# Optimization experiments

Hardware: AMD Instinct MI355X
Metric: run time of the kernel (lower is better)

The kernel has to match this reference:

```python
import jax, jax.numpy as jnp
import numpy as np

B, D, G, K, NP = 8, 1024, 32, 64, 1024


def setup_inputs() -> dict:
    key = jax.random.key(0)
    ks = jax.random.split(key, 7)
    x = jax.random.normal(ks[0], (B, NP, D), jnp.float32)
    weights = jax.random.uniform(ks[1], (B, G), jnp.float32)
    xopt = jax.random.normal(ks[2], (B, D), jnp.float32)
    R = jax.random.normal(ks[3], (K, K), jnp.float32) / np.sqrt(K).astype(np.float32)
    group_indices = jax.random.randint(ks[4], (B, G, K), 0, D)
    valid_mask = jax.random.randint(ks[5], (B, G, K), 0, 2).astype(bool)
    group_counts = jax.random.randint(ks[6], (B,), 1, G + 1)
    return dict(x=x, weights=weights, xopt=xopt, R=R,
                group_indices=group_indices, valid_mask=valid_mask,
                group_counts=group_counts)


def reference(x, weights, xopt, R, group_indices, valid_mask, group_counts):
    Bb, NPp, Dd = x.shape
    Gg, Kk = group_indices.shape[1], group_indices.shape[2]
    # elliptic coefficients 1e6**linspace(0,1,K), a deterministic buffer
    coeffs = jnp.asarray(1.0e6, x.dtype) ** jnp.linspace(0.0, 1.0, Kk).astype(x.dtype)
    z = x - xopt[:, None, :]                                   # (B,NP,D)
    # gather per-group sub-vectors without materializing (B,G,NP,D):
    # zb: (NP,D), ib: (G,K) -> zb[:, ib]: (NP,G,K)
    z_sub = jax.vmap(lambda zb, ib: zb[:, ib])(z, group_indices)  # (B,NP,G,K)
    z_sub = jnp.transpose(z_sub, (0, 2, 1, 3))                 # (B,G,NP,K)
    # per-group small rotation
    z_rot = jnp.einsum('bgnk,kl->bgnl', z_sub, R)              # (B,G,NP,K)
    # mask invalid dims of each group, elliptic weighted sum over K
    masked_coeffs = jnp.where(valid_mask[:, :, None, :], coeffs[None, None, None, :],
                              jnp.zeros((), x.dtype))          # (B,G,NP->bcast,K)
    elliptic_vals = jnp.sum(masked_coeffs * z_rot * z_rot, axis=-1)  # (B,G,NP)
    # mask invalid groups, weighted reduce over groups
    group_valid = (jnp.arange(Gg)[None, :] < group_counts[:, None]).astype(x.dtype)  # (B,G)
    fitness = jnp.einsum('bgn,bg->bn', elliptic_vals, weights * group_valid)  # (B,NP)
    return fitness
```

## Files before the change

### kernel.cpp

```cpp
#include <hip/hip_runtime.h>

typedef _Float16 half8  __attribute__((ext_vector_type(8)));
typedef _Float16 half4h __attribute__((ext_vector_type(4)));
typedef float    f32x4  __attribute__((ext_vector_type(4)));

#define B_     8
#define D_     1024
#define G_     32
#define K_     64
#define NP_    1024
#define ROWS   32
#define TPB    1024
#define STRIDE 1028

__global__ __launch_bounds__(TPB) void fitness(
    const float* __restrict__ x,
    const float* __restrict__ weights,
    const float* __restrict__ xopt,
    const float* __restrict__ R,
    const int* __restrict__ gidx,
    const int* __restrict__ mask,
    const int* __restrict__ counts,
    float* __restrict__ out) {
  __shared__ _Float16 zh[ROWS * STRIDE];
  __shared__ int      gli[G_ * K_];
  __shared__ _Float16 Rb[8 * 512];
  __shared__ float    wcs[G_ * K_];
  __shared__ float    redrow[ROWS];

  const int tile = blockIdx.x;
  const int b    = blockIdx.y;
  const int t    = threadIdx.x;
  const int cnt  = counts[b];

  gli[t]        = gidx[b * (G_ * K_) + t];
  gli[t + 1024] = gidx[b * (G_ * K_) + 1024 + t];

  {
    const float C = 19.931568569324174f / 63.0f;
#pragma unroll
    for (int r = 0; r < 2; ++r) {
      int idx = t + r * 1024;
      int g = idx >> 6, l = idx & 63;
      bool v = (g < cnt) && (mask[b * (G_ * K_) + idx] != 0);
      wcs[idx] = v ? weights[b * G_ + g] * exp2f((float)l * C) : 0.0f;
    }
  }

  {
    int pos  = t * 4;
    int frag = pos >> 9, rem = pos & 511;
    int lane = rem >> 3, j0 = rem & 7;
    int kt = frag >> 2, nt = frag & 3;
    int quad = lane >> 4, ln = lane & 15;
    half4h rv;
#pragma unroll
    for (int e = 0; e < 4; ++e) {
      int k = kt * 32 + quad * 8 + j0 + e;
      rv[e] = (_Float16)R[k * K_ + nt * 16 + ln];
    }
    *(half4h*)(Rb + pos) = rv;
  }

  if (t < ROWS) redrow[t] = 0.0f;

  {
    const float4* x4  = (const float4*)(x + ((size_t)(b * NP_ + tile * ROWS)) * D_);
    const float4* xo4 = (const float4*)(xopt + b * D_);
    const int col4 = t & 255;
    float4 xo = xo4[col4];
#pragma unroll
    for (int j = 0; j < (ROWS * 256) / TPB; ++j) {
      int row = (t >> 8) + 4 * j;
      float4 xv = x4[row * 256 + col4];
      half4h hv;
      hv[0] = (_Float16)(xv.x - xo.x);
      hv[1] = (_Float16)(xv.y - xo.y);
      hv[2] = (_Float16)(xv.z - xo.z);
      hv[3] = (_Float16)(xv.w - xo.w);
      *(half4h*)(zh + row * STRIDE + col4 * 4) = hv;
    }
  }
  __syncthreads();

  const int wv   = t >> 6;
  const int lane = t & 63;
  const int quad = lane >> 4;
  const int ln   = lane & 15;
  const int items = 2 * cnt;

  const half8* rbf = (const half8*)Rb;

  for (int i = wv; i < items; i += 16) {
    const int g     = i >> 1;
    const int mtile = i & 1;

    const int* gp = gli + g * K_ + quad * 8;
    int4 i0 = *(const int4*)(gp);
    int4 i1 = *(const int4*)(gp + 4);
    int4 i2 = *(const int4*)(gp + 32);
    int4 i3 = *(const int4*)(gp + 36);
    const _Float16* zr = zh + (mtile * 16 + ln) * STRIDE;
    half8 a0, a1;
    a0[0] = zr[i0.x]; a0[1] = zr[i0.y]; a0[2] = zr[i0.z]; a0[3] = zr[i0.w];
    a0[4] = zr[i1.x]; a0[5] = zr[i1.y]; a0[6] = zr[i1.z]; a0[7] = zr[i1.w];
    a1[0] = zr[i2.x]; a1[1] = zr[i2.y]; a1[2] = zr[i2.z]; a1[3] = zr[i2.w];
    a1[4] = zr[i3.x]; a1[5] = zr[i3.y]; a1[6] = zr[i3.z]; a1[7] = zr[i3.w];

    f32x4 c0 = {0.f, 0.f, 0.f, 0.f}, c1 = c0, c2 = c0, c3 = c0;
    c0 = __builtin_amdgcn_mfma_f32_16x16x32_f16(a0, rbf[0 * 64 + lane], c0, 0, 0, 0);
    c1 = __builtin_amdgcn_mfma_f32_16x16x32_f16(a0, rbf[1 * 64 + lane], c1, 0, 0, 0);
    c2 = __builtin_amdgcn_mfma_f32_16x16x32_f16(a0, rbf[2 * 64 + lane], c2, 0, 0, 0);
    c3 = __builtin_amdgcn_mfma_f32_16x16x32_f16(a0, rbf[3 * 64 + lane], c3, 0, 0, 0);
    c0 = __builtin_amdgcn_mfma_f32_16x16x32_f16(a1, rbf[4 * 64 + lane], c0, 0, 0, 0);
    c1 = __builtin_amdgcn_mfma_f32_16x16x32_f16(a1, rbf[5 * 64 + lane], c1, 0, 0, 0);
    c2 = __builtin_amdgcn_mfma_f32_16x16x32_f16(a1, rbf[6 * 64 + lane], c2, 0, 0, 0);
    c3 = __builtin_amdgcn_mfma_f32_16x16x32_f16(a1, rbf[7 * 64 + lane], c3, 0, 0, 0);

    const float* wg = wcs + g * K_ + ln;
    float w0 = wg[0], w1 = wg[16], w2 = wg[32], w3 = wg[48];
    float q0, q1, q2, q3;
    q0 = w0 * c0[0] * c0[0] + w1 * c1[0] * c1[0] + w2 * c2[0] * c2[0] + w3 * c3[0] * c3[0];
    q1 = w0 * c0[1] * c0[1] + w1 * c1[1] * c1[1] + w2 * c2[1] * c2[1] + w3 * c3[1] * c3[1];
    q2 = w0 * c0[2] * c0[2] + w1 * c1[2] * c1[2] + w2 * c2[2] * c2[2] + w3 * c3[2] * c3[2];
    q3 = w0 * c0[3] * c0[3] + w1 * c1[3] * c1[3] + w2 * c2[3] * c2[3] + w3 * c3[3] * c3[3];

#pragma unroll
    for (int off = 1; off < 16; off <<= 1) {
      q0 += __shfl_xor(q0, off);
      q1 += __shfl_xor(q1, off);
      q2 += __shfl_xor(q2, off);
      q3 += __shfl_xor(q3, off);
    }
    if (ln == 0) {
      float* rr = redrow + mtile * 16 + quad * 4;
      atomicAdd(rr + 0, q0);
      atomicAdd(rr + 1, q1);
      atomicAdd(rr + 2, q2);
      atomicAdd(rr + 3, q3);
    }
  }
  __syncthreads();

  if (t < ROWS) out[b * NP_ + tile * ROWS + t] = redrow[t];
}

extern "C" void kernel_launch(void* const* d_in, const int* in_sizes, int n_in,
                              void* d_out, int out_size, void* d_ws, size_t ws_size,
                              hipStream_t stream) {
  const float* x       = (const float*)d_in[0];
  const float* weights = (const float*)d_in[1];
  const float* xopt    = (const float*)d_in[2];
  const float* R       = (const float*)d_in[3];
  const int*   gidx    = (const int*)d_in[4];
  const int*   mask    = (const int*)d_in[5];
  const int*   counts  = (const int*)d_in[6];
  float*       out     = (float*)d_out;

  fitness<<<dim3(NP_ / ROWS, B_), dim3(TPB), 0, stream>>>(
      x, weights, xopt, R, gidx, mask, counts, out);
}
```

Measured before the change: 90.17 us.

## Hoist weight/R prep into separate kernel, halve tile size, keep R in registers

```diff
diff --git a/kernel.cpp b/kernel.cpp
--- a/kernel.cpp
+++ b/kernel.cpp
@@ -9,23 +9,44 @@
 #define G_     32
 #define K_     64
 #define NP_    1024
-#define ROWS   32
-#define TPB    1024
+#define ROWS   16
+#define TPB    512
 #define STRIDE 1028
 
-__global__ __launch_bounds__(TPB) void fitness(
+
+__global__ void prep(const float* __restrict__ weights,
+                     const int* __restrict__ mask,
+                     const int* __restrict__ counts,
+                     const float* __restrict__ R,
+                     float* __restrict__ wcs,
+                     _Float16* __restrict__ rbf) {
+  int idx = blockIdx.x * 256 + threadIdx.x;
+  int bg = idx >> 6, l = idx & 63;
+  int b = bg >> 5, g = bg & 31;
+  const float C = 19.931568569324174f / 63.0f;
+  bool v = (g < counts[b]) && (mask[idx] != 0);
+  wcs[idx] = v ? weights[bg] * exp2f((float)l * C) : 0.0f;
+
+  if (idx < 8 * 512) {
+    int frag = idx >> 9, rem = idx & 511;
+    int lane = rem >> 3, j = rem & 7;
+    int kt = frag >> 2, nt = frag & 3;
+    int quad = lane >> 4, ln = lane & 15;
+    int k = kt * 32 + quad * 8 + j;
+    rbf[idx] = (_Float16)R[k * K_ + nt * 16 + ln];
+  }
+}
+
+__global__ __launch_bounds__(TPB, 4) void fitness(
     const float* __restrict__ x,
-    const float* __restrict__ weights,
     const float* __restrict__ xopt,
-    const float* __restrict__ R,
     const int* __restrict__ gidx,
-    const int* __restrict__ mask,
     const int* __restrict__ counts,
+    const float* __restrict__ wcs,
+    const _Float16* __restrict__ rbf,
     float* __restrict__ out) {
   __shared__ _Float16 zh[ROWS * STRIDE];
   __shared__ int      gli[G_ * K_];
-  __shared__ _Float16 Rb[8 * 512];
-  __shared__ float    wcs[G_ * K_];
   __shared__ float    redrow[ROWS];
 
   const int tile = blockIdx.x;
@@ -33,35 +54,7 @@
   const int t    = threadIdx.x;
   const int cnt  = counts[b];
 
-  gli[t]        = gidx[b * (G_ * K_) + t];
-  gli[t + 1024] = gidx[b * (G_ * K_) + 1024 + t];
-
-  {
-    const float C = 19.931568569324174f / 63.0f;
-#pragma unroll
-    for (int r = 0; r < 2; ++r) {
-      int idx = t + r * 1024;
-      int g = idx >> 6, l = idx & 63;
-      bool v = (g < cnt) && (mask[b * (G_ * K_) + idx] != 0);
-      wcs[idx] = v ? weights[b * G_ + g] * exp2f((float)l * C) : 0.0f;
-    }
-  }
-
-  {
-    int pos  = t * 4;
-    int frag = pos >> 9, rem = pos & 511;
-    int lane = rem >> 3, j0 = rem & 7;
-    int kt = frag >> 2, nt = frag & 3;
-    int quad = lane >> 4, ln = lane & 15;
-    half4h rv;
-#pragma unroll
-    for (int e = 0; e < 4; ++e) {
-      int k = kt * 32 + quad * 8 + j0 + e;
-      rv[e] = (_Float16)R[k * K_ + nt * 16 + ln];
-    }
-    *(half4h*)(Rb + pos) = rv;
-  }
-
+  ((int4*)gli)[t] = ((const int4*)(gidx + b * (G_ * K_)))[t];
   if (t < ROWS) redrow[t] = 0.0f;
 
   {
@@ -70,8 +63,8 @@
     const int col4 = t & 255;
     float4 xo = xo4[col4];
 #pragma unroll
-    for (int j = 0; j < (ROWS * 256) / TPB; ++j) {
-      int row = (t >> 8) + 4 * j;
+    for (int j = 0; j < 8; ++j) {
+      int row = (t >> 8) + 2 * j;
       float4 xv = x4[row * 256 + col4];
       half4h hv;
       hv[0] = (_Float16)(xv.x - xo.x);
@@ -81,26 +74,30 @@
       *(half4h*)(zh + row * STRIDE + col4 * 4) = hv;
     }
   }
-  __syncthreads();
 
   const int wv   = t >> 6;
   const int lane = t & 63;
   const int quad = lane >> 4;
   const int ln   = lane & 15;
-  const int items = 2 * cnt;
 
-  const half8* rbf = (const half8*)Rb;
+  half8 rb[8];
+#pragma unroll
+  for (int f = 0; f < 8; ++f) rb[f] = *(const half8*)(rbf + f * 512 + lane * 8);
 
-  for (int i = wv; i < items; i += 16) {
-    const int g     = i >> 1;
-    const int mtile = i & 1;
+  __syncthreads();
+
+  const _Float16* zr = zh + ln * STRIDE;
+  float q0 = 0.f, q1 = 0.f, q2 = 0.f, q3 = 0.f;
+
+  for (int g = wv; g < cnt; g += 8) {
+    const float* wg = wcs + (b * G_ + g) * K_ + ln;
+    float w0 = wg[0], w1 = wg[16], w2 = wg[32], w3 = wg[48];
 
     const int* gp = gli + g * K_ + quad * 8;
     int4 i0 = *(const int4*)(gp);
     int4 i1 = *(const int4*)(gp + 4);
     int4 i2 = *(const int4*)(gp + 32);
     int4 i3 = *(const int4*)(gp + 36);
-    const _Float16* zr = zh + (mtile * 16 + ln) * STRIDE;
     half8 a0, a1;
     a0[0] = zr[i0.x]; a0[1] = zr[i0.y]; a0[2] = zr[i0.z]; a0[3] = zr[i0.w];
     a0[4] = zr[i1.x]; a0[5] = zr[i1.y]; a0[6] = zr[i1.z]; a0[7] = zr[i1.w];
@@ -108,37 +105,34 @@
     a1[4] = zr[i3.x]; a1[5] = zr[i3.y]; a1[6] = zr[i3.z]; a1[7] = zr[i3.w];
 
     f32x4 c0 = {0.f, 0.f, 0.f, 0.f}, c1 = c0, c2 = c0, c3 = c0;
-    c0 = __builtin_amdgcn_mfma_f32_16x16x32_f16(a0, rbf[0 * 64 + lane], c0, 0, 0, 0);
-    c1 = __builtin_amdgcn_mfma_f32_16x16x32_f16(a0, rbf[1 * 64 + lane], c1, 0, 0, 0);
-    c2 = __builtin_amdgcn_mfma_f32_16x16x32_f16(a0, rbf[2 * 64 + lane], c2, 0, 0, 0);
-    c3 = __builtin_amdgcn_mfma_f32_16x16x32_f16(a0, rbf[3 * 64 + lane], c3, 0, 0, 0);
-    c0 = __builtin_amdgcn_mfma_f32_16x16x32_f16(a1, rbf[4 * 64 + lane], c0, 0, 0, 0);
-    c1 = __builtin_amdgcn_mfma_f32_16x16x32_f16(a1, rbf[5 * 64 + lane], c1, 0, 0, 0);
-    c2 = __builtin_amdgcn_mfma_f32_16x16x32_f16(a1, rbf[6 * 64 + lane], c2, 0, 0, 0);
-    c3 = __builtin_amdgcn_mfma_f32_16x16x32_f16(a1, rbf[7 * 64 + lane], c3, 0, 0, 0);
+    c0 = __builtin_amdgcn_mfma_f32_16x16x32_f16(a0, rb[0], c0, 0, 0, 0);
+    c1 = __builtin_amdgcn_mfma_f32_16x16x32_f16(a0, rb[1], c1, 0, 0, 0);
+    c2 = __builtin_amdgcn_mfma_f32_16x16x32_f16(a0, rb[2], c2, 0, 0, 0);
+    c3 = __builtin_amdgcn_mfma_f32_16x16x32_f16(a0, rb[3], c3, 0, 0, 0);
+    c0 = __builtin_amdgcn_mfma_f32_16x16x32_f16(a1, rb[4], c0, 0, 0, 0);
+    c1 = __builtin_amdgcn_mfma_f32_16x16x32_f16(a1, rb[5], c1, 0, 0, 0);
+    c2 = __builtin_amdgcn_mfma_f32_16x16x32_f16(a1, rb[6], c2, 0, 0, 0);
+    c3 = __builtin_amdgcn_mfma_f32_16x16x32_f16(a1, rb[7], c3, 0, 0, 0);
 
-    const float* wg = wcs + g * K_ + ln;
-    float w0 = wg[0], w1 = wg[16], w2 = wg[32], w3 = wg[48];
-    float q0, q1, q2, q3;
-    q0 = w0 * c0[0] * c0[0] + w1 * c1[0] * c1[0] + w2 * c2[0] * c2[0] + w3 * c3[0] * c3[0];
-    q1 = w0 * c0[1] * c0[1] + w1 * c1[1] * c1[1] + w2 * c2[1] * c2[1] + w3 * c3[1] * c3[1];
-    q2 = w0 * c0[2] * c0[2] + w1 * c1[2] * c1[2] + w2 * c2[2] * c2[2] + w3 * c3[2] * c3[2];
-    q3 = w0 * c0[3] * c0[3] + w1 * c1[3] * c1[3] + w2 * c2[3] * c2[3] + w3 * c3[3] * c3[3];
+    q0 += w0 * c0[0] * c0[0] + w1 * c1[0] * c1[0] + w2 * c2[0] * c2[0] + w3 * c3[0] * c3[0];
+    q1 += w0 * c0[1] * c0[1] + w1 * c1[1] * c1[1] + w2 * c2[1] * c2[1] + w3 * c3[1] * c3[1];
+    q2 += w0 * c0[2] * c0[2] + w1 * c1[2] * c1[2] + w2 * c2[2] * c2[2] + w3 * c3[2] * c3[2];
+    q3 += w0 * c0[3] * c0[3] + w1 * c1[3] * c1[3] + w2 * c2[3] * c2[3] + w3 * c3[3] * c3[3];
+  }
 
 #pragma unroll
-    for (int off = 1; off < 16; off <<= 1) {
-      q0 += __shfl_xor(q0, off);
-      q1 += __shfl_xor(q1, off);
-      q2 += __shfl_xor(q2, off);
-      q3 += __shfl_xor(q3, off);
-    }
-    if (ln == 0) {
-      float* rr = redrow + mtile * 16 + quad * 4;
-      atomicAdd(rr + 0, q0);
-      atomicAdd(rr + 1, q1);
-      atomicAdd(rr + 2, q2);
-      atomicAdd(rr + 3, q3);
-    }
+  for (int off = 1; off < 16; off <<= 1) {
+    q0 += __shfl_xor(q0, off);
+    q1 += __shfl_xor(q1, off);
+    q2 += __shfl_xor(q2, off);
+    q3 += __shfl_xor(q3, off);
+  }
+  if (ln == 0 && wv < cnt) {
+    float* rr = redrow + quad * 4;
+    atomicAdd(rr + 0, q0);
+    atomicAdd(rr + 1, q1);
+    atomicAdd(rr + 2, q2);
+    atomicAdd(rr + 3, q3);
   }
   __syncthreads();
 
@@ -157,6 +151,10 @@
   const int*   counts  = (const int*)d_in[6];
   float*       out     = (float*)d_out;
 
+  float*    wcs = (float*)d_ws;
+  _Float16* rbf = (_Float16*)((char*)d_ws + B_ * G_ * K_ * sizeof(float));
+
+  prep<<<dim3(64), dim3(256), 0, stream>>>(weights, mask, counts, R, wcs, rbf);
   fitness<<<dim3(NP_ / ROWS, B_), dim3(TPB), 0, stream>>>(
-      x, weights, xopt, R, gidx, mask, counts, out);
+      x, xopt, gidx, counts, wcs, rbf, out);
 }
```

After: 88.92 us. Within noise of the previous version (-1.4%).
